# Kernel tuning notes

Hardware: AMD Instinct MI355X
Metric: run time of the kernel (lower is better)

Reference implementation:

```python
import jax, jax.numpy as jnp
import numpy as np

TREND_SCALING = 0.6
DETAIL_PRESERVATION = 0.85
SPIKE_THRESHOLD = 3.5
SPIKE_DAMPING = 0.35
ITERATIONS = 2
EPS = 1e-6


def _smooth(x, kernel):
    # x: [B, C, L], kernel: [1, 1, W] (normalized box filter)
    W = kernel.shape[-1]
    pad = W // 2
    xp = jnp.pad(x, ((0, 0), (0, 0), (pad, pad)), mode='reflect')
    C = x.shape[1]
    w = jnp.broadcast_to(kernel, (C, 1, W))  # depthwise weight [C, 1, W]
    return jax.lax.conv_general_dilated(
        xp, w, window_strides=(1,), padding='VALID',
        dimension_numbers=('NCH', 'OIH', 'NCH'), feature_group_count=C)


def setup_inputs() -> dict:
    key = jax.random.key(0)
    x = jax.random.normal(key, (16, 32, 65536), dtype=jnp.float32)
    # buffers from __init__ with base_window=5
    detail_kernel = jnp.ones((1, 1, 5), dtype=jnp.float32) / 5.0
    trend_kernel = jnp.ones((1, 1, 11), dtype=jnp.float32) / 11.0
    return {"x": x, "detail_kernel": detail_kernel, "trend_kernel": trend_kernel}


def reference(x, detail_kernel, trend_kernel):
    current = x.astype(jnp.float32)
    for _ in range(ITERATIONS):
        trend = _smooth(current, trend_kernel)
        local = _smooth(current, detail_kernel)
        residual = current - local
        # torch .std uses Bessel's correction (ddof=1)
        scale = jnp.maximum(jnp.std(residual, axis=-1, keepdims=True, ddof=1), EPS)
        threshold = scale * SPIKE_THRESHOLD
        residual = jnp.where(jnp.abs(residual) > threshold,
                             residual * SPIKE_DAMPING, residual)
        residual = residual * DETAIL_PRESERVATION
        combined = (1.0 - TREND_SCALING) * local + TREND_SCALING * trend
        current = combined + residual
    return current
```

## Files before the change

kernel.cpp:

```cpp
#include <hip/hip_runtime.h>
#include <math.h>

#define LROW   65536
#define NROWS  512
#define CHUNK  4096
#define NCH    (LROW / CHUNK)
#define NT     256
#define EPT    (CHUNK / NT)
#define HALO   5
#define NELEM  (CHUNK + 2 * HALO)

#define TREND_SCALING       0.6f
#define DETAIL_PRESERVATION 0.85f
#define SPIKE_THRESHOLD     3.5f
#define SPIKE_DAMPING       0.35f
#define EPSV                1e-6f

#define PART_BYTES (NROWS * NCH * 2 * 8)

__device__ __forceinline__ int sw(int i) { return i + (i >> 4); }

template <bool STASH>
__global__ __launch_bounds__(NT) void k_sum(const float* __restrict__ src,
                                            const float* __restrict__ k5,
                                            double* __restrict__ partials,
                                            float* __restrict__ edges) {
    __shared__ float buf[NELEM + (NELEM >> 4) + 2];
    const int bid = blockIdx.x;
    const int row = bid >> 4;
    const int c = bid & (NCH - 1);
    const size_t rowBase = (size_t)row * LROW;
    const int cStart = c * CHUNK;
    const int tid = threadIdx.x;
    const float w5 = k5[0];

    const float4* src4 = (const float4*)(src + rowBase + cStart);
    for (int j4 = tid; j4 < CHUNK / 4; j4 += NT) {
        float4 t4 = src4[j4];
        int l = j4 * 4 + HALO;
        buf[sw(l)] = t4.x;
        buf[sw(l + 1)] = t4.y;
        buf[sw(l + 2)] = t4.z;
        buf[sw(l + 3)] = t4.w;
    }
    if (tid < 2 * HALO) {
        int j = (tid < HALO) ? tid : (CHUNK + tid);
        int g = cStart - HALO + j;
        g = (g < 0) ? -g : (g >= LROW ? 2 * LROW - 2 - g : g);
        buf[sw(j)] = src[rowBase + g];
    }
    __syncthreads();

    if (STASH && tid < 10) {
        int l = (tid < 5) ? (HALO + tid) : (CHUNK + tid - 5);
        edges[(size_t)bid * 10 + tid] = buf[sw(l)];
    }

    float v[EPT + 2 * HALO];
    const int base = tid * EPT;
#pragma unroll
    for (int j = 0; j < EPT + 2 * HALO; j++) v[j] = buf[sw(base + j)];

    double s = 0.0, q = 0.0;
#pragma unroll
    for (int k = 0; k < EPT; k++) {
        float lac = 0.f;
#pragma unroll
        for (int d = 0; d < 5; d++) lac = fmaf(v[k + 3 + d], w5, lac);
        float r = v[k + HALO] - lac;
        s += (double)r;
        q += (double)r * (double)r;
    }

    __shared__ double rs[NT], rq[NT];
    rs[tid] = s;
    rq[tid] = q;
    __syncthreads();
    for (int off = NT / 2; off > 0; off >>= 1) {
        if (tid < off) {
            rs[tid] += rs[tid + off];
            rq[tid] += rq[tid + off];
        }
        __syncthreads();
    }
    if (tid == 0) {
        partials[(size_t)bid * 2] = rs[0];
        partials[(size_t)bid * 2 + 1] = rq[0];
    }
}

__global__ void k_red(const double* __restrict__ partials, float* __restrict__ thr) {
    int r = blockIdx.x * blockDim.x + threadIdx.x;
    if (r >= NROWS) return;
    double s = 0.0, q = 0.0;
    for (int c = 0; c < NCH; c++) {
        s += partials[(size_t)(r * NCH + c) * 2];
        q += partials[(size_t)(r * NCH + c) * 2 + 1];
    }
    const double N = (double)LROW;
    double var = (q - s * s / N) / (N - 1.0);
    if (var < 0.0) var = 0.0;
    float sd = (float)sqrt(var);
    float scale = fmaxf(sd, EPSV);
    thr[r] = scale * SPIKE_THRESHOLD;
}

template <bool USE_EDGES>
__global__ __launch_bounds__(NT) void k_apply(const float* src, float* dst,
                                              const float* k5, const float* k11,
                                              const float* thr, const float* edges) {
    __shared__ float buf[NELEM + (NELEM >> 4) + 2];
    const int bid = blockIdx.x;
    const int row = bid >> 4;
    const int c = bid & (NCH - 1);
    const size_t rowBase = (size_t)row * LROW;
    const int cStart = c * CHUNK;
    const int tid = threadIdx.x;
    const float w5 = k5[0];
    const float w11 = k11[0];
    const float th = thr[row];

    const float4* src4 = (const float4*)(src + rowBase + cStart);
    for (int j4 = tid; j4 < CHUNK / 4; j4 += NT) {
        float4 t4 = src4[j4];
        int l = j4 * 4 + HALO;
        buf[sw(l)] = t4.x;
        buf[sw(l + 1)] = t4.y;
        buf[sw(l + 2)] = t4.z;
        buf[sw(l + 3)] = t4.w;
    }
    if (!USE_EDGES) {
        if (tid < 2 * HALO) {
            int j = (tid < HALO) ? tid : (CHUNK + tid);
            int g = cStart - HALO + j;
            g = (g < 0) ? -g : (g >= LROW ? 2 * LROW - 2 - g : g);
            buf[sw(j)] = src[rowBase + g];
        }
        __syncthreads();
    } else {
        __syncthreads();
        if (tid < HALO) {
            float val;
            if (c > 0)
                val = edges[((size_t)bid - 1) * 10 + 5 + tid];
            else
                val = buf[sw(10 - tid)];
            buf[sw(tid)] = val;
        } else if (tid < 2 * HALO) {
            int k = tid - HALO;
            float val;
            if (c < NCH - 1)
                val = edges[((size_t)bid + 1) * 10 + k];
            else
                val = buf[sw(CHUNK + 3 - k)];
            buf[sw(CHUNK + HALO + k)] = val;
        }
        __syncthreads();
    }

    float v[EPT + 2 * HALO];
    const int base = tid * EPT;
#pragma unroll
    for (int j = 0; j < EPT + 2 * HALO; j++) v[j] = buf[sw(base + j)];

    float o[EPT];
#pragma unroll
    for (int k = 0; k < EPT; k++) {
        float lac = 0.f, tac = 0.f;
#pragma unroll
        for (int d = 0; d < 5; d++) lac = fmaf(v[k + 3 + d], w5, lac);
#pragma unroll
        for (int d = 0; d < 11; d++) tac = fmaf(v[k + d], w11, tac);
        float cur = v[k + HALO];
        float r = cur - lac;
        r = (fabsf(r) > th) ? r * SPIKE_DAMPING : r;
        float comb = (1.0f - TREND_SCALING) * lac + TREND_SCALING * tac;
        o[k] = comb + DETAIL_PRESERVATION * r;
    }

    float4* dst4 = (float4*)(dst + rowBase + cStart + base);
#pragma unroll
    for (int k4 = 0; k4 < EPT / 4; k4++) {
        dst4[k4] = make_float4(o[4 * k4], o[4 * k4 + 1], o[4 * k4 + 2], o[4 * k4 + 3]);
    }
}

extern "C" void kernel_launch(void* const* d_in, const int* in_sizes, int n_in,
                              void* d_out, int out_size, void* d_ws, size_t ws_size,
                              hipStream_t stream) {
    const float* x = (const float*)d_in[0];
    const float* k5 = (const float*)d_in[1];
    const float* k11 = (const float*)d_in[2];
    float* out = (float*)d_out;
    char* ws = (char*)d_ws;
    double* partials = (double*)ws;
    float* thr = (float*)(ws + PART_BYTES);
    float* edges = (float*)(ws + PART_BYTES + 4096);

    dim3 grid(NROWS * NCH), block(NT);

    hipLaunchKernelGGL((k_sum<false>), grid, block, 0, stream, x, k5, partials, edges);
    hipLaunchKernelGGL(k_red, dim3(2), dim3(NT), 0, stream, partials, thr);
    hipLaunchKernelGGL((k_apply<false>), grid, block, 0, stream, x, out, k5, k11, thr, edges);

    hipLaunchKernelGGL((k_sum<true>), grid, block, 0, stream, out, k5, partials, edges);
    hipLaunchKernelGGL(k_red, dim3(2), dim3(NT), 0, stream, partials, thr);
    hipLaunchKernelGGL((k_apply<true>), grid, block, 0, stream, out, out, k5, k11, thr, edges);
}
```

Measured before the change: 364.2 us.

## Fuse second-iteration statistics into first apply pass and inline threshold reduction

The first apply kernel now loads a wider halo, recomputes neighbour boundary outputs, and accumulates the second iteration's residual sum and sum of squares directly from its register outputs. This removes a separate full read pass over the intermediate array. The second reduction kernel is folded into the final apply kernel, which derives the threshold from the per-chunk partials. Block reductions switch from a shared-memory tree to wave shuffles. In exchange, the first apply kernel does extra boundary recomputation and holds more registers and shared memory.

```diff
diff --git a/kernel.cpp b/kernel.cpp
--- a/kernel.cpp
+++ b/kernel.cpp
@@ -8,7 +8,9 @@
 #define NT     256
 #define EPT    (CHUNK / NT)
 #define HALO   5
+#define HALO2  7
 #define NELEM  (CHUNK + 2 * HALO)
+#define NELEM2 (CHUNK + 2 * HALO2)
 
 #define TREND_SCALING       0.6f
 #define DETAIL_PRESERVATION 0.85f
@@ -20,12 +22,11 @@
 
 __device__ __forceinline__ int sw(int i) { return i + (i >> 4); }
 
-template <bool STASH>
 __global__ __launch_bounds__(NT) void k_sum(const float* __restrict__ src,
                                             const float* __restrict__ k5,
-                                            double* __restrict__ partials,
-                                            float* __restrict__ edges) {
+                                            double* __restrict__ partials) {
     __shared__ float buf[NELEM + (NELEM >> 4) + 2];
+    __shared__ double wsd[2 * (NT / 64)];
     const int bid = blockIdx.x;
     const int row = bid >> 4;
     const int c = bid & (NCH - 1);
@@ -51,11 +52,6 @@
     }
     __syncthreads();
 
-    if (STASH && tid < 10) {
-        int l = (tid < 5) ? (HALO + tid) : (CHUNK + tid - 5);
-        edges[(size_t)bid * 10 + tid] = buf[sw(l)];
-    }
-
     float v[EPT + 2 * HALO];
     const int base = tid * EPT;
 #pragma unroll
@@ -71,21 +67,20 @@
         s += (double)r;
         q += (double)r * (double)r;
     }
-
-    __shared__ double rs[NT], rq[NT];
-    rs[tid] = s;
-    rq[tid] = q;
-    __syncthreads();
-    for (int off = NT / 2; off > 0; off >>= 1) {
-        if (tid < off) {
-            rs[tid] += rs[tid + off];
-            rq[tid] += rq[tid + off];
-        }
-        __syncthreads();
-    }
+#pragma unroll
+    for (int off = 32; off > 0; off >>= 1) {
+        s += __shfl_xor(s, off);
+        q += __shfl_xor(q, off);
+    }
+    const int lane = tid & 63, wid = tid >> 6;
+    if (lane == 0) { wsd[wid] = s; wsd[wid + NT / 64] = q; }
+    __syncthreads();
     if (tid == 0) {
-        partials[(size_t)bid * 2] = rs[0];
-        partials[(size_t)bid * 2 + 1] = rq[0];
+        double S = 0.0, Q = 0.0;
+#pragma unroll
+        for (int w = 0; w < NT / 64; w++) { S += wsd[w]; Q += wsd[w + NT / 64]; }
+        partials[(size_t)bid * 2] = S;
+        partials[(size_t)bid * 2 + 1] = Q;
     }
 }
 
@@ -105,11 +100,17 @@
     thr[r] = scale * SPIKE_THRESHOLD;
 }
 
-template <bool USE_EDGES>
-__global__ __launch_bounds__(NT) void k_apply(const float* src, float* dst,
-                                              const float* k5, const float* k11,
-                                              const float* thr, const float* edges) {
-    __shared__ float buf[NELEM + (NELEM >> 4) + 2];
+__global__ __launch_bounds__(NT) void k_apply_fuse(const float* __restrict__ src,
+                                                   float* __restrict__ dst,
+                                                   const float* __restrict__ k5,
+                                                   const float* __restrict__ k11,
+                                                   const float* __restrict__ thr,
+                                                   double* __restrict__ partials,
+                                                   float* __restrict__ edges) {
+    __shared__ float buf[NELEM2 + (NELEM2 >> 4) + 2];
+    __shared__ float2 oF[NT], oL[NT];
+    __shared__ float eB[4];
+    __shared__ double wsd[2 * (NT / 64)];
     const int bid = blockIdx.x;
     const int row = bid >> 4;
     const int c = bid & (NCH - 1);
@@ -123,45 +124,24 @@
     const float4* src4 = (const float4*)(src + rowBase + cStart);
     for (int j4 = tid; j4 < CHUNK / 4; j4 += NT) {
         float4 t4 = src4[j4];
-        int l = j4 * 4 + HALO;
+        int l = j4 * 4 + HALO2;
         buf[sw(l)] = t4.x;
         buf[sw(l + 1)] = t4.y;
         buf[sw(l + 2)] = t4.z;
         buf[sw(l + 3)] = t4.w;
     }
-    if (!USE_EDGES) {
-        if (tid < 2 * HALO) {
-            int j = (tid < HALO) ? tid : (CHUNK + tid);
-            int g = cStart - HALO + j;
-            g = (g < 0) ? -g : (g >= LROW ? 2 * LROW - 2 - g : g);
-            buf[sw(j)] = src[rowBase + g];
-        }
-        __syncthreads();
-    } else {
-        __syncthreads();
-        if (tid < HALO) {
-            float val;
-            if (c > 0)
-                val = edges[((size_t)bid - 1) * 10 + 5 + tid];
-            else
-                val = buf[sw(10 - tid)];
-            buf[sw(tid)] = val;
-        } else if (tid < 2 * HALO) {
-            int k = tid - HALO;
-            float val;
-            if (c < NCH - 1)
-                val = edges[((size_t)bid + 1) * 10 + k];
-            else
-                val = buf[sw(CHUNK + 3 - k)];
-            buf[sw(CHUNK + HALO + k)] = val;
-        }
-        __syncthreads();
-    }
+    if (tid < 2 * HALO2) {
+        int j = (tid < HALO2) ? tid : (CHUNK + tid);
+        int g = cStart - HALO2 + j;
+        g = (g < 0) ? -g : (g >= LROW ? 2 * LROW - 2 - g : g);
+        buf[sw(j)] = src[rowBase + g];
+    }
+    __syncthreads();
 
     float v[EPT + 2 * HALO];
     const int base = tid * EPT;
 #pragma unroll
-    for (int j = 0; j < EPT + 2 * HALO; j++) v[j] = buf[sw(base + j)];
+    for (int j = 0; j < EPT + 2 * HALO; j++) v[j] = buf[sw(base + 2 + j)];
 
     float o[EPT];
 #pragma unroll
@@ -178,7 +158,158 @@
         o[k] = comb + DETAIL_PRESERVATION * r;
     }
 
+    if (tid < 4) {
+        const int p = (tid < 2) ? (tid - 2) : (CHUNK + tid - 2);
+        float ve[11];
+#pragma unroll
+        for (int j = 0; j < 11; j++) ve[j] = buf[sw(p + 2 + j)];
+        float lac = 0.f, tac = 0.f;
+#pragma unroll
+        for (int d = 0; d < 5; d++) lac = fmaf(ve[3 + d], w5, lac);
+#pragma unroll
+        for (int d = 0; d < 11; d++) tac = fmaf(ve[d], w11, tac);
+        float cur = ve[5];
+        float r = cur - lac;
+        r = (fabsf(r) > th) ? r * SPIKE_DAMPING : r;
+        float comb = (1.0f - TREND_SCALING) * lac + TREND_SCALING * tac;
+        eB[tid] = comb + DETAIL_PRESERVATION * r;
+    }
+    oF[tid] = make_float2(o[0], o[1]);
+    oL[tid] = make_float2(o[EPT - 2], o[EPT - 1]);
+
+    if (tid == 0) {
+#pragma unroll
+        for (int j = 0; j < 5; j++) edges[(size_t)bid * 10 + j] = o[j];
+    }
+    if (tid == NT - 1) {
+#pragma unroll
+        for (int j = 0; j < 5; j++) edges[(size_t)bid * 10 + 5 + j] = o[EPT - 5 + j];
+    }
+
     float4* dst4 = (float4*)(dst + rowBase + cStart + base);
+#pragma unroll
+    for (int k4 = 0; k4 < EPT / 4; k4++)
+        dst4[k4] = make_float4(o[4 * k4], o[4 * k4 + 1], o[4 * k4 + 2], o[4 * k4 + 3]);
+
+    __syncthreads();
+
+    const float2 lp = (tid == 0) ? make_float2(eB[0], eB[1]) : oL[tid - 1];
+    const float2 rp = (tid == NT - 1) ? make_float2(eB[2], eB[3]) : oF[tid + 1];
+
+    float oe[EPT + 4];
+    oe[0] = lp.x;
+    oe[1] = lp.y;
+#pragma unroll
+    for (int k = 0; k < EPT; k++) oe[2 + k] = o[k];
+    oe[EPT + 2] = rp.x;
+    oe[EPT + 3] = rp.y;
+
+    double s = 0.0, q = 0.0;
+#pragma unroll
+    for (int k = 0; k < EPT; k++) {
+        float lac = 0.f;
+#pragma unroll
+        for (int d = 0; d < 5; d++) lac = fmaf(oe[k + d], w5, lac);
+        float r = oe[k + 2] - lac;
+        s += (double)r;
+        q += (double)r * (double)r;
+    }
+#pragma unroll
+    for (int off = 32; off > 0; off >>= 1) {
+        s += __shfl_xor(s, off);
+        q += __shfl_xor(q, off);
+    }
+    const int lane = tid & 63, wid = tid >> 6;
+    if (lane == 0) { wsd[wid] = s; wsd[wid + NT / 64] = q; }
+    __syncthreads();
+    if (tid == 0) {
+        double S = 0.0, Q = 0.0;
+#pragma unroll
+        for (int w = 0; w < NT / 64; w++) { S += wsd[w]; Q += wsd[w + NT / 64]; }
+        partials[(size_t)bid * 2] = S;
+        partials[(size_t)bid * 2 + 1] = Q;
+    }
+}
+
+__global__ __launch_bounds__(NT) void k_apply2(float* io,
+                                               const float* __restrict__ k5,
+                                               const float* __restrict__ k11,
+                                               const double* __restrict__ partials,
+                                               const float* __restrict__ edges) {
+    __shared__ float buf[NELEM + (NELEM >> 4) + 2];
+    __shared__ double prow[2 * NCH];
+    const int bid = blockIdx.x;
+    const int row = bid >> 4;
+    const int c = bid & (NCH - 1);
+    const size_t rowBase = (size_t)row * LROW;
+    const int cStart = c * CHUNK;
+    const int tid = threadIdx.x;
+    const float w5 = k5[0];
+    const float w11 = k11[0];
+
+    if (tid < 2 * NCH) prow[tid] = partials[(size_t)row * (2 * NCH) + tid];
+
+    const float4* src4 = (const float4*)(io + rowBase + cStart);
+    for (int j4 = tid; j4 < CHUNK / 4; j4 += NT) {
+        float4 t4 = src4[j4];
+        int l = j4 * 4 + HALO;
+        buf[sw(l)] = t4.x;
+        buf[sw(l + 1)] = t4.y;
+        buf[sw(l + 2)] = t4.z;
+        buf[sw(l + 3)] = t4.w;
+    }
+    __syncthreads();
+    if (tid < HALO) {
+        float val;
+        if (c > 0)
+            val = edges[((size_t)bid - 1) * 10 + 5 + tid];
+        else
+            val = buf[sw(10 - tid)];
+        buf[sw(tid)] = val;
+    } else if (tid < 2 * HALO) {
+        int k = tid - HALO;
+        float val;
+        if (c < NCH - 1)
+            val = edges[((size_t)bid + 1) * 10 + k];
+        else
+            val = buf[sw(CHUNK + 3 - k)];
+        buf[sw(CHUNK + HALO + k)] = val;
+    }
+    __syncthreads();
+
+    double s = 0.0, q = 0.0;
+#pragma unroll
+    for (int cc = 0; cc < NCH; cc++) {
+        s += prow[2 * cc];
+        q += prow[2 * cc + 1];
+    }
+    const double N = (double)LROW;
+    double var = (q - s * s / N) / (N - 1.0);
+    if (var < 0.0) var = 0.0;
+    float sd = (float)sqrt(var);
+    const float th = fmaxf(sd, EPSV) * SPIKE_THRESHOLD;
+
+    float v[EPT + 2 * HALO];
+    const int base = tid * EPT;
+#pragma unroll
+    for (int j = 0; j < EPT + 2 * HALO; j++) v[j] = buf[sw(base + j)];
+
+    float o[EPT];
+#pragma unroll
+    for (int k = 0; k < EPT; k++) {
+        float lac = 0.f, tac = 0.f;
+#pragma unroll
+        for (int d = 0; d < 5; d++) lac = fmaf(v[k + 3 + d], w5, lac);
+#pragma unroll
+        for (int d = 0; d < 11; d++) tac = fmaf(v[k + d], w11, tac);
+        float cur = v[k + HALO];
+        float r = cur - lac;
+        r = (fabsf(r) > th) ? r * SPIKE_DAMPING : r;
+        float comb = (1.0f - TREND_SCALING) * lac + TREND_SCALING * tac;
+        o[k] = comb + DETAIL_PRESERVATION * r;
+    }
+
+    float4* dst4 = (float4*)(io + rowBase + cStart + base);
 #pragma unroll
     for (int k4 = 0; k4 < EPT / 4; k4++) {
         dst4[k4] = make_float4(o[4 * k4], o[4 * k4 + 1], o[4 * k4 + 2], o[4 * k4 + 3]);
@@ -188,6 +319,7 @@
 extern "C" void kernel_launch(void* const* d_in, const int* in_sizes, int n_in,
                               void* d_out, int out_size, void* d_ws, size_t ws_size,
                               hipStream_t stream) {
+    (void)in_sizes; (void)n_in; (void)out_size; (void)ws_size;
     const float* x = (const float*)d_in[0];
     const float* k5 = (const float*)d_in[1];
     const float* k11 = (const float*)d_in[2];
@@ -199,11 +331,9 @@
 
     dim3 grid(NROWS * NCH), block(NT);
 
-    hipLaunchKernelGGL((k_sum<false>), grid, block, 0, stream, x, k5, partials, edges);
+    hipLaunchKernelGGL(k_sum, grid, block, 0, stream, x, k5, partials);
     hipLaunchKernelGGL(k_red, dim3(2), dim3(NT), 0, stream, partials, thr);
-    hipLaunchKernelGGL((k_apply<false>), grid, block, 0, stream, x, out, k5, k11, thr, edges);
-
-    hipLaunchKernelGGL((k_sum<true>), grid, block, 0, stream, out, k5, partials, edges);
-    hipLaunchKernelGGL(k_red, dim3(2), dim3(NT), 0, stream, partials, thr);
-    hipLaunchKernelGGL((k_apply<true>), grid, block, 0, stream, out, out, k5, k11, thr, edges);
-}
+    hipLaunchKernelGGL(k_apply_fuse, grid, block, 0, stream, x, out, k5, k11, thr,
+                       partials, edges);
+    hipLaunchKernelGGL(k_apply2, grid, block, 0, stream, out, k5, k11, partials, edges);
+}
```

Result: faster. 336.6 us (-7.6%).
